# Kernel optimization log

Hardware: AMD Instinct MI355X
Metric: run time of the kernel (lower is better)

The kernel has to match this reference:

```python
import jax, jax.numpy as jnp
import numpy as np

N_NODES = 100000
N_EDGES = 6400000
NUM_FEATURES = 128
NUM_CLASSES = 10


def _gcn_norm(edge_index, num_nodes):
    # PyG GCNConv default: add self-loops, symmetric normalization
    src, dst = edge_index[0], edge_index[1]
    loop = jnp.arange(num_nodes, dtype=src.dtype)
    src = jnp.concatenate([src, loop])
    dst = jnp.concatenate([dst, loop])
    deg = jax.ops.segment_sum(jnp.ones_like(dst, dtype=jnp.float32), dst,
                              num_segments=num_nodes)
    dinv = jnp.where(deg > 0, jax.lax.rsqrt(deg), 0.0)
    norm = dinv[src] * dinv[dst]  # [E + N]
    return src, dst, norm


def _gcn_conv(x, W, b, src, dst, norm, num_nodes):
    h = x @ W                              # [N, out] small feature matmul
    msg = h[src] * norm[:, None]           # gather + per-edge scale
    agg = jax.ops.segment_sum(msg, dst, num_segments=num_nodes)  # scatter-add
    return agg + b


def setup_inputs() -> dict:
    key = jax.random.key(0)
    ks = jax.random.split(key, 10)
    x = jax.random.normal(ks[0], (N_NODES, NUM_FEATURES), dtype=jnp.float32)
    edge_index = jax.random.randint(ks[1], (2, N_EDGES), 0, N_NODES, dtype=jnp.int64)

    def glorot(k, shape):
        lim = np.sqrt(6.0 / (shape[0] + shape[1]))
        return jax.random.uniform(k, shape, jnp.float32, -lim, lim)

    return {
        "x": x,
        "edge_index": edge_index,
        "W1": glorot(ks[2], (NUM_FEATURES, 4)), "b1": jnp.zeros((4,), jnp.float32),
        "W2": glorot(ks[3], (4, 4)),            "b2": jnp.zeros((4,), jnp.float32),
        "W3": glorot(ks[4], (4, 2)),            "b3": jnp.zeros((2,), jnp.float32),
        "Wc": glorot(ks[5], (2, NUM_CLASSES)),  "bc": jnp.zeros((NUM_CLASSES,), jnp.float32),
    }


def reference(x, edge_index, W1, b1, W2, b2, W3, b3, Wc, bc):
    num_nodes = x.shape[0]
    src, dst, norm = _gcn_norm(edge_index, num_nodes)
    h = jnp.tanh(_gcn_conv(x, W1, b1, src, dst, norm, num_nodes))
    h = jnp.tanh(_gcn_conv(h, W2, b2, src, dst, norm, num_nodes))
    h = jnp.tanh(_gcn_conv(h, W3, b3, src, dst, norm, num_nodes))
    out = h @ Wc + bc
    return out, h
```

## Files before the change

kernel.cpp:

```cpp
#include <hip/hip_runtime.h>
#include <hip/hip_bf16.h>
#include <stdint.h>

#define N_NODES 100000
#define N_EDGES 6400000

#define NPB 128
#define NBKT 782
#define CAP 10752
#define SORT_CAP 9216
#define OUT_CAP (SORT_CAP + NPB * 3)
#define BIN_CHUNK 16384
#define BIN_THREADS 1024
#define SORT_THREADS 1024
#define SORT_V4 3
#define NBIN_BLOCKS ((N_EDGES + BIN_CHUNK - 1) / BIN_CHUNK)


__global__ __launch_bounds__(1024) void k_bin(const void* __restrict__ ei,
                                              int* __restrict__ gcur,
                                              unsigned* __restrict__ perm1) {
  __shared__ unsigned staging[BIN_CHUNK];
  __shared__ int lcnt[1024];
  __shared__ int combo[1024];
  __shared__ int wsum[16];
  __shared__ int s_tot;
  __shared__ int s_th[3];
  __shared__ int s_is64;
  int t = threadIdx.x;
  lcnt[t] = 0;
  if (t < 64) {
    unsigned hv = ((const unsigned*)ei)[2 * t + 1];
    unsigned long long m = __ballot(hv != 0u);
    if (t == 0) s_is64 = (m == 0ull);
  }
  __syncthreads();
  int is64 = s_is64;
  size_t e0 = (size_t)blockIdx.x * BIN_CHUNK;
  int n = (int)(((e0 + BIN_CHUNK) <= N_EDGES) ? BIN_CHUNK : (N_EDGES - e0));

  if (is64) {
    const long long* e = (const long long*)ei;
    for (int k = 2 * t; k < n; k += 2048) {
      uint4 dp = *(const uint4*)(e + (size_t)N_EDGES + e0 + k);
      if (dp.x < N_NODES) atomicAdd(&lcnt[dp.x >> 7], 1);
      if (dp.z < N_NODES) atomicAdd(&lcnt[dp.z >> 7], 1);
    }
  } else {
    const unsigned* e = (const unsigned*)ei;
    for (int k = 4 * t; k < n; k += 4096) {
      uint4 dq = *(const uint4*)(e + (size_t)N_EDGES + e0 + k);
      if (dq.x < N_NODES) atomicAdd(&lcnt[dq.x >> 7], 1);
      if (dq.y < N_NODES) atomicAdd(&lcnt[dq.y >> 7], 1);
      if (dq.z < N_NODES) atomicAdd(&lcnt[dq.z >> 7], 1);
      if (dq.w < N_NODES) atomicAdd(&lcnt[dq.w >> 7], 1);
    }
  }
  __syncthreads();
  int c = lcnt[t];
  int lane = t & 63, w = t >> 6;
  int incl = c;
#pragma unroll
  for (int o = 1; o < 64; o <<= 1) {
    int u = __shfl_up(incl, o);
    if (lane >= o) incl += u;
  }
  if (lane == 63) wsum[w] = incl;
  __syncthreads();
  int wb = 0;
  for (int i = 0; i < w; ++i) wb += wsum[i];
  int excl = wb + incl - c;
  int gb = c ? atomicAdd(&gcur[t], c) : 0;
  lcnt[t] = excl;
  combo[t] = gb - excl;
  if (t == 256) s_th[0] = excl;
  if (t == 512) s_th[1] = excl;
  if (t == 768) s_th[2] = excl;
  if (t == 1023) s_tot = excl + c;
  __syncthreads();
  if (is64) {
    const long long* e = (const long long*)ei;
    for (int k = 2 * t; k < n; k += 2048) {
      uint4 sp = *(const uint4*)(e + e0 + k);
      uint4 dp = *(const uint4*)(e + (size_t)N_EDGES + e0 + k);
      if (sp.x < N_NODES && dp.x < N_NODES) {
        int p = atomicAdd(&lcnt[dp.x >> 7], 1);
        staging[p] = sp.x | ((dp.x & (NPB - 1u)) << 17) | (((dp.x >> 7) & 255u) << 24);
      }
      if (sp.z < N_NODES && dp.z < N_NODES) {
        int p = atomicAdd(&lcnt[dp.z >> 7], 1);
        staging[p] = sp.z | ((dp.z & (NPB - 1u)) << 17) | (((dp.z >> 7) & 255u) << 24);
      }
    }
  } else {
    const unsigned* e = (const unsigned*)ei;
    for (int k = 4 * t; k < n; k += 4096) {
      uint4 sq = *(const uint4*)(e + e0 + k);
      uint4 dq = *(const uint4*)(e + (size_t)N_EDGES + e0 + k);
      if (sq.x < N_NODES && dq.x < N_NODES) {
        int p = atomicAdd(&lcnt[dq.x >> 7], 1);
        staging[p] = sq.x | ((dq.x & (NPB - 1u)) << 17) | (((dq.x >> 7) & 255u) << 24);
      }
      if (sq.y < N_NODES && dq.y < N_NODES) {
        int p = atomicAdd(&lcnt[dq.y >> 7], 1);
        staging[p] = sq.y | ((dq.y & (NPB - 1u)) << 17) | (((dq.y >> 7) & 255u) << 24);
      }
      if (sq.z < N_NODES && dq.z < N_NODES) {
        int p = atomicAdd(&lcnt[dq.z >> 7], 1);
        staging[p] = sq.z | ((dq.z & (NPB - 1u)) << 17) | (((dq.z >> 7) & 255u) << 24);
      }
      if (sq.w < N_NODES && dq.w < N_NODES) {
        int p = atomicAdd(&lcnt[dq.w >> 7], 1);
        staging[p] = sq.w | ((dq.w & (NPB - 1u)) << 17) | (((dq.w >> 7) & 255u) << 24);
      }
    }
  }
  __syncthreads();
  int tot = s_tot, th0 = s_th[0], th1 = s_th[1], th2 = s_th[2];
  for (int j = t; j < tot; j += 1024) {
    unsigned r = staging[j];
    int hi = (j >= th0) + (j >= th1) + (j >= th2);
    int b = (int)(r >> 24) | (hi << 8);
    int o = combo[b] + j;
    if (o < CAP) perm1[(size_t)b * CAP + o] = r;
  }
}

__global__ __launch_bounds__(1024) void k_sort(const int* __restrict__ gcur,
                                               const unsigned* __restrict__ perm1,
                                               unsigned* __restrict__ perm2,
                                               int2* __restrict__ offdeg,
                                               float* __restrict__ dinv) {
  __shared__ __align__(16) unsigned outbuf[OUT_CAP];
  __shared__ int h[NPB];
  __shared__ int wsum2[2];
  __shared__ int s_tot;
  int b = blockIdx.x, t = threadIdx.x;
  if (t < NPB) h[t] = 0;
  __syncthreads();
  int cnt = min(gcur[b], SORT_CAP);
  int base = b * CAP;
#pragma unroll
  for (int i = 0; i < SORT_V4; ++i) {
    int j = 4 * t + 4096 * i;
    if (j < cnt) {
      uint4 q = *(const uint4*)(perm1 + base + j);
      atomicAdd(&h[(q.x >> 17) & (NPB - 1)], 1);
      if (j + 1 < cnt) atomicAdd(&h[(q.y >> 17) & (NPB - 1)], 1);
      if (j + 2 < cnt) atomicAdd(&h[(q.z >> 17) & (NPB - 1)], 1);
      if (j + 3 < cnt) atomicAdd(&h[(q.w >> 17) & (NPB - 1)], 1);
    }
  }
  __syncthreads();
  int degb = 0, degs4 = 0, incl = 0;
  if (t < NPB) {
    degb = h[t];
    degs4 = (degb + 3) & ~3;
    incl = degs4;
    int lane = t & 63;
#pragma unroll
    for (int o = 1; o < 64; o <<= 1) {
      int u = __shfl_up(incl, o);
      if (lane >= o) incl += u;
    }
    if (lane == 63) wsum2[t >> 6] = incl;
  }
  __syncthreads();
  int excl4 = 0;
  if (t < NPB) {
    excl4 = (t >= 64 ? wsum2[0] : 0) + incl - degs4;
    int node = b * NPB + t;
    if (node < N_NODES) {
      offdeg[node] = make_int2(base + excl4, degb);
      float dd = (float)degb + 1.0f;
      float y = rsqrtf(dd);
      y = y * (1.5f - 0.5f * dd * y * y);
      dinv[node] = y;
    }
    if (t == NPB - 1) s_tot = excl4 + degs4;
  }
  __syncthreads();
  if (t < NPB) h[t] = excl4;
  __syncthreads();
#pragma unroll
  for (int i = 0; i < SORT_V4; ++i) {
    int j = 4 * t + 4096 * i;
    if (j < cnt) {
      uint4 q = *(const uint4*)(perm1 + base + j);
      { int p = atomicAdd(&h[(q.x >> 17) & (NPB - 1)], 1); outbuf[p] = q.x & 0x1FFFF; }
      if (j + 1 < cnt) { int p = atomicAdd(&h[(q.y >> 17) & (NPB - 1)], 1); outbuf[p] = q.y & 0x1FFFF; }
      if (j + 2 < cnt) { int p = atomicAdd(&h[(q.z >> 17) & (NPB - 1)], 1); outbuf[p] = q.z & 0x1FFFF; }
      if (j + 3 < cnt) { int p = atomicAdd(&h[(q.w >> 17) & (NPB - 1)], 1); outbuf[p] = q.w & 0x1FFFF; }
    }
  }
  __syncthreads();
  int tot = s_tot;
#pragma unroll
  for (int i = 0; i < SORT_V4; ++i) {
    int j = 4 * t + 4096 * i;
    if (j < tot)
      *(uint4*)(perm2 + base + j) = *(const uint4*)(outbuf + j);
  }
}

__global__ __launch_bounds__(256) void k_mm1(const float* __restrict__ x,
                                             const float* __restrict__ W1,
                                             const float* __restrict__ dinv,
                                             float* __restrict__ hs1) {
  int gid = blockIdx.x * blockDim.x + threadIdx.x;
  int node = gid >> 6;
  int lane = threadIdx.x & 63;
  if (node >= N_NODES) return;
  float2 v = ((const float2*)x)[(size_t)node * 64 + lane];
  float4 w0 = ((const float4*)W1)[2 * lane];
  float4 w1 = ((const float4*)W1)[2 * lane + 1];
  float a0 = v.x * w0.x + v.y * w1.x;
  float a1 = v.x * w0.y + v.y * w1.y;
  float a2 = v.x * w0.z + v.y * w1.z;
  float a3 = v.x * w0.w + v.y * w1.w;
#pragma unroll
  for (int off = 32; off > 0; off >>= 1) {
    a0 += __shfl_down(a0, off);
    a1 += __shfl_down(a1, off);
    a2 += __shfl_down(a2, off);
    a3 += __shfl_down(a3, off);
  }
  if (lane == 0) {
    float d = dinv[node];
    ((float4*)hs1)[node] = make_float4(d * a0, d * a1, d * a2, d * a3);
  }
}


__global__ __launch_bounds__(256) void k_l1(const int2* __restrict__ offdeg,
                                            const unsigned* __restrict__ perm2,
                                            const float* __restrict__ hs1,
                                            const float* __restrict__ dinv,
                                            const float* __restrict__ W2,
                                            const float* __restrict__ b1,
                                            float* __restrict__ hs2) {
  int node = blockIdx.x * 16 + (threadIdx.x >> 4);
  int l = threadIdx.x & 15;
  int2 od = offdeg[node];
  int base = od.x, d = od.y;
  float a0 = 0, a1 = 0, a2 = 0, a3 = 0;
  for (int j = 4 * l; j + 4 <= d; j += 64) {
    uint4 s = *(const uint4*)(perm2 + base + j);
    float4 v0 = ((const float4*)hs1)[s.x];
    float4 v1 = ((const float4*)hs1)[s.y];
    float4 v2 = ((const float4*)hs1)[s.z];
    float4 v3 = ((const float4*)hs1)[s.w];
    a0 += v0.x + v1.x + v2.x + v3.x;
    a1 += v0.y + v1.y + v2.y + v3.y;
    a2 += v0.z + v1.z + v2.z + v3.z;
    a3 += v0.w + v1.w + v2.w + v3.w;
  }
  int rb = d & ~3;
  if (l < d - rb) {
    float4 v = ((const float4*)hs1)[perm2[base + rb + l]];
    a0 += v.x; a1 += v.y; a2 += v.z; a3 += v.w;
  }
#pragma unroll
  for (int o = 8; o > 0; o >>= 1) {
    a0 += __shfl_down(a0, o); a1 += __shfl_down(a1, o);
    a2 += __shfl_down(a2, o); a3 += __shfl_down(a3, o);
  }
  if (l == 0) {
    float dn = dinv[node];
    float4 hl = ((const float4*)hs1)[node];
    float t0 = tanhf(dn * (a0 + hl.x) + b1[0]);
    float t1 = tanhf(dn * (a1 + hl.y) + b1[1]);
    float t2 = tanhf(dn * (a2 + hl.z) + b1[2]);
    float t3 = tanhf(dn * (a3 + hl.w) + b1[3]);
    float4 r;
    r.x = dn * (t0 * W2[0] + t1 * W2[4] + t2 * W2[8]  + t3 * W2[12]);
    r.y = dn * (t0 * W2[1] + t1 * W2[5] + t2 * W2[9]  + t3 * W2[13]);
    r.z = dn * (t0 * W2[2] + t1 * W2[6] + t2 * W2[10] + t3 * W2[14]);
    r.w = dn * (t0 * W2[3] + t1 * W2[7] + t2 * W2[11] + t3 * W2[15]);
    ((float4*)hs2)[node] = r;
  }
}

__global__ __launch_bounds__(256) void k_l2(const int2* __restrict__ offdeg,
                                            const unsigned* __restrict__ perm2,
                                            const float* __restrict__ hs2,
                                            const float* __restrict__ dinv,
                                            const float* __restrict__ W3,
                                            const float* __restrict__ b2,
                                            float* __restrict__ hs3) {
  int node = blockIdx.x * 16 + (threadIdx.x >> 4);
  int l = threadIdx.x & 15;
  int2 od = offdeg[node];
  int base = od.x, d = od.y;
  float a0 = 0, a1 = 0, a2 = 0, a3 = 0;
  for (int j = 4 * l; j + 4 <= d; j += 64) {
    uint4 s = *(const uint4*)(perm2 + base + j);
    float4 v0 = ((const float4*)hs2)[s.x];
    float4 v1 = ((const float4*)hs2)[s.y];
    float4 v2 = ((const float4*)hs2)[s.z];
    float4 v3 = ((const float4*)hs2)[s.w];
    a0 += v0.x + v1.x + v2.x + v3.x;
    a1 += v0.y + v1.y + v2.y + v3.y;
    a2 += v0.z + v1.z + v2.z + v3.z;
    a3 += v0.w + v1.w + v2.w + v3.w;
  }
  int rb = d & ~3;
  if (l < d - rb) {
    float4 v = ((const float4*)hs2)[perm2[base + rb + l]];
    a0 += v.x; a1 += v.y; a2 += v.z; a3 += v.w;
  }
#pragma unroll
  for (int o = 8; o > 0; o >>= 1) {
    a0 += __shfl_down(a0, o); a1 += __shfl_down(a1, o);
    a2 += __shfl_down(a2, o); a3 += __shfl_down(a3, o);
  }
  if (l == 0) {
    float dn = dinv[node];
    float4 hl = ((const float4*)hs2)[node];
    float t0 = tanhf(dn * (a0 + hl.x) + b2[0]);
    float t1 = tanhf(dn * (a1 + hl.y) + b2[1]);
    float t2 = tanhf(dn * (a2 + hl.z) + b2[2]);
    float t3 = tanhf(dn * (a3 + hl.w) + b2[3]);
    float2 r;
    r.x = dn * (t0 * W3[0] + t1 * W3[2] + t2 * W3[4] + t3 * W3[6]);
    r.y = dn * (t0 * W3[1] + t1 * W3[3] + t2 * W3[5] + t3 * W3[7]);
    ((float2*)hs3)[node] = r;
  }
}

__global__ __launch_bounds__(256) void k_l3(const int2* __restrict__ offdeg,
                                            const unsigned* __restrict__ perm2,
                                            const float* __restrict__ hs3,
                                            const float* __restrict__ dinv,
                                            const float* __restrict__ Wc,
                                            const float* __restrict__ bc,
                                            const float* __restrict__ b3,
                                            float* __restrict__ out) {
  int node = blockIdx.x * 16 + (threadIdx.x >> 4);
  int l = threadIdx.x & 15;
  int2 od = offdeg[node];
  int base = od.x, d = od.y;
  float a0 = 0, a1 = 0;
  for (int j = 4 * l; j + 4 <= d; j += 64) {
    uint4 s = *(const uint4*)(perm2 + base + j);
    float2 v0 = ((const float2*)hs3)[s.x];
    float2 v1 = ((const float2*)hs3)[s.y];
    float2 v2 = ((const float2*)hs3)[s.z];
    float2 v3 = ((const float2*)hs3)[s.w];
    a0 += v0.x + v1.x + v2.x + v3.x;
    a1 += v0.y + v1.y + v2.y + v3.y;
  }
  int rb = d & ~3;
  if (l < d - rb) {
    float2 v = ((const float2*)hs3)[perm2[base + rb + l]];
    a0 += v.x; a1 += v.y;
  }
#pragma unroll
  for (int o = 8; o > 0; o >>= 1) {
    a0 += __shfl_xor(a0, o); a1 += __shfl_xor(a1, o);
  }
  float dn = dinv[node];
  float2 hl = ((const float2*)hs3)[node];
  float t0 = tanhf(dn * (a0 + hl.x) + b3[0]);
  float t1 = tanhf(dn * (a1 + hl.y) + b3[1]);
  if (l < 10)
    out[(size_t)node * 10 + l] = t0 * Wc[l] + t1 * Wc[10 + l] + bc[l];
  else if (l == 10)
    out[(size_t)N_NODES * 10 + 2 * node + 0] = t0;
  else if (l == 11)
    out[(size_t)N_NODES * 10 + 2 * node + 1] = t1;
}

extern "C" void kernel_launch(void* const* d_in, const int* in_sizes, int n_in,
                              void* d_out, int out_size, void* d_ws, size_t ws_size,
                              hipStream_t stream) {
  const float* x  = (const float*)d_in[0];
  const void*  ei = d_in[1];
  const float* W1 = (const float*)d_in[2];
  const float* b1 = (const float*)d_in[3];
  const float* W2 = (const float*)d_in[4];
  const float* b2 = (const float*)d_in[5];
  const float* W3 = (const float*)d_in[6];
  const float* b3 = (const float*)d_in[7];
  const float* Wc = (const float*)d_in[8];
  const float* bc = (const float*)d_in[9];
  float* out = (float*)d_out;

  const size_t N = N_NODES;
  float* base = (float*)d_ws;
  float* dinv = base;
  float* hs1  = base + N;
  float* hs2  = base + 5 * N;
  float* hs3  = base + 9 * N;
  int2*  offdeg = (int2*)(base + 11 * N);
  int*   gcur = (int*)(base + 13 * N);
  unsigned* perm1 = (unsigned*)(base + 13 * N + 2048);
  unsigned* perm2 = perm1 + (size_t)NBKT * CAP;

  hipMemsetAsync(gcur, 0, 1024 * sizeof(int), stream);
  k_bin<<<NBIN_BLOCKS, BIN_THREADS, 0, stream>>>(ei, gcur, perm1);
  k_sort<<<NBKT, SORT_THREADS, 0, stream>>>(gcur, perm1, perm2, offdeg, dinv);
  k_mm1<<<(N_NODES * 64) / 256, 256, 0, stream>>>(x, W1, dinv, hs1);

  const int LB = N_NODES / 16;
  k_l1<<<LB, 256, 0, stream>>>(offdeg, perm2, hs1, dinv, W2, b1, hs2);
  k_l2<<<LB, 256, 0, stream>>>(offdeg, perm2, hs2, dinv, W3, b2, hs3);
  k_l3<<<LB, 256, 0, stream>>>(offdeg, perm2, hs3, dinv, Wc, bc, b3, out);
}
```

Baseline: 281.6 us.

## Fuse matmul and three GCN layers into one persistent kernel with grid barriers

Replaces four separate launches (x@W1 and three aggregation layers) with a single persistent kernel of 1024 blocks. The blocks use grid-stride loops and synchronize between stages through atomic-counter grid barriers held in workspace, which is zeroed by the extended memset. This removes three kernel launch gaps and their tail effects. In exchange it relies on all 1024 blocks being co-resident to avoid deadlock, and it reduces per-stage parallelism and latency hiding compared with the fully oversubscribed grids.

```diff
diff --git a/kernel.cpp b/kernel.cpp
--- a/kernel.cpp
+++ b/kernel.cpp
@@ -15,6 +15,9 @@
 #define SORT_THREADS 1024
 #define SORT_V4 3
 #define NBIN_BLOCKS ((N_EDGES + BIN_CHUNK - 1) / BIN_CHUNK)
+
+#define FUSE_BLOCKS 1024
+#define FUSE_THREADS 256
 
 
 __global__ __launch_bounds__(1024) void k_bin(const void* __restrict__ ei,
@@ -203,172 +206,176 @@
   }
 }
 
-__global__ __launch_bounds__(256) void k_mm1(const float* __restrict__ x,
-                                             const float* __restrict__ W1,
-                                             const float* __restrict__ dinv,
-                                             float* __restrict__ hs1) {
-  int gid = blockIdx.x * blockDim.x + threadIdx.x;
-  int node = gid >> 6;
-  int lane = threadIdx.x & 63;
-  if (node >= N_NODES) return;
-  float2 v = ((const float2*)x)[(size_t)node * 64 + lane];
-  float4 w0 = ((const float4*)W1)[2 * lane];
-  float4 w1 = ((const float4*)W1)[2 * lane + 1];
-  float a0 = v.x * w0.x + v.y * w1.x;
-  float a1 = v.x * w0.y + v.y * w1.y;
-  float a2 = v.x * w0.z + v.y * w1.z;
-  float a3 = v.x * w0.w + v.y * w1.w;
-#pragma unroll
-  for (int off = 32; off > 0; off >>= 1) {
-    a0 += __shfl_down(a0, off);
-    a1 += __shfl_down(a1, off);
-    a2 += __shfl_down(a2, off);
-    a3 += __shfl_down(a3, off);
-  }
-  if (lane == 0) {
-    float d = dinv[node];
-    ((float4*)hs1)[node] = make_float4(d * a0, d * a1, d * a2, d * a3);
-  }
+__device__ __forceinline__ void grid_barrier(int* bar, int id, int nb) {
+  __syncthreads();
+  if (threadIdx.x == 0) {
+    __threadfence();
+    __hip_atomic_fetch_add(&bar[id], 1, __ATOMIC_ACQ_REL, __HIP_MEMORY_SCOPE_AGENT);
+    while (__hip_atomic_load(&bar[id], __ATOMIC_ACQUIRE, __HIP_MEMORY_SCOPE_AGENT) < nb) {}
+    __threadfence();
+  }
+  __syncthreads();
 }
 
-
-__global__ __launch_bounds__(256) void k_l1(const int2* __restrict__ offdeg,
-                                            const unsigned* __restrict__ perm2,
-                                            const float* __restrict__ hs1,
-                                            const float* __restrict__ dinv,
-                                            const float* __restrict__ W2,
-                                            const float* __restrict__ b1,
-                                            float* __restrict__ hs2) {
-  int node = blockIdx.x * 16 + (threadIdx.x >> 4);
-  int l = threadIdx.x & 15;
-  int2 od = offdeg[node];
-  int base = od.x, d = od.y;
-  float a0 = 0, a1 = 0, a2 = 0, a3 = 0;
-  for (int j = 4 * l; j + 4 <= d; j += 64) {
-    uint4 s = *(const uint4*)(perm2 + base + j);
-    float4 v0 = ((const float4*)hs1)[s.x];
-    float4 v1 = ((const float4*)hs1)[s.y];
-    float4 v2 = ((const float4*)hs1)[s.z];
-    float4 v3 = ((const float4*)hs1)[s.w];
-    a0 += v0.x + v1.x + v2.x + v3.x;
-    a1 += v0.y + v1.y + v2.y + v3.y;
-    a2 += v0.z + v1.z + v2.z + v3.z;
-    a3 += v0.w + v1.w + v2.w + v3.w;
-  }
-  int rb = d & ~3;
-  if (l < d - rb) {
-    float4 v = ((const float4*)hs1)[perm2[base + rb + l]];
-    a0 += v.x; a1 += v.y; a2 += v.z; a3 += v.w;
-  }
-#pragma unroll
-  for (int o = 8; o > 0; o >>= 1) {
-    a0 += __shfl_down(a0, o); a1 += __shfl_down(a1, o);
-    a2 += __shfl_down(a2, o); a3 += __shfl_down(a3, o);
-  }
-  if (l == 0) {
+__global__ __launch_bounds__(256, 4) void k_fused(
+    const float* __restrict__ x,  const float* __restrict__ W1,
+    const int2* __restrict__ offdeg, const unsigned* __restrict__ perm2,
+    const float* __restrict__ dinv,
+    const float* __restrict__ b1, const float* __restrict__ W2,
+    const float* __restrict__ b2, const float* __restrict__ W3,
+    const float* __restrict__ b3, const float* __restrict__ Wc,
+    const float* __restrict__ bc,
+    float* __restrict__ hs1, float* __restrict__ hs2,
+    float* __restrict__ hs3, float* __restrict__ out,
+    int* __restrict__ bar) {
+  const int tid = blockIdx.x * FUSE_THREADS + threadIdx.x;
+
+  {
+    int wave = tid >> 6;
+    int lane = threadIdx.x & 63;
+    const int nwaves = (FUSE_BLOCKS * FUSE_THREADS) >> 6;
+    float4 w0 = ((const float4*)W1)[2 * lane];
+    float4 w1 = ((const float4*)W1)[2 * lane + 1];
+    for (int node = wave; node < N_NODES; node += nwaves) {
+      float2 v = ((const float2*)x)[(size_t)node * 64 + lane];
+      float a0 = v.x * w0.x + v.y * w1.x;
+      float a1 = v.x * w0.y + v.y * w1.y;
+      float a2 = v.x * w0.z + v.y * w1.z;
+      float a3 = v.x * w0.w + v.y * w1.w;
+#pragma unroll
+      for (int off = 32; off > 0; off >>= 1) {
+        a0 += __shfl_down(a0, off);
+        a1 += __shfl_down(a1, off);
+        a2 += __shfl_down(a2, off);
+        a3 += __shfl_down(a3, off);
+      }
+      if (lane == 0) {
+        float d = dinv[node];
+        ((float4*)hs1)[node] = make_float4(d * a0, d * a1, d * a2, d * a3);
+      }
+    }
+  }
+  grid_barrier(bar, 0, FUSE_BLOCKS);
+
+  const int slot = tid >> 4;
+  const int l = threadIdx.x & 15;
+  const int nslots = (FUSE_BLOCKS * FUSE_THREADS) >> 4;
+
+  for (int node = slot; node < N_NODES; node += nslots) {
+    int2 od = offdeg[node];
+    int base = od.x, d = od.y;
+    float a0 = 0, a1 = 0, a2 = 0, a3 = 0;
+    for (int j = 4 * l; j + 4 <= d; j += 64) {
+      uint4 s = *(const uint4*)(perm2 + base + j);
+      float4 v0 = ((const float4*)hs1)[s.x];
+      float4 v1 = ((const float4*)hs1)[s.y];
+      float4 v2 = ((const float4*)hs1)[s.z];
+      float4 v3 = ((const float4*)hs1)[s.w];
+      a0 += v0.x + v1.x + v2.x + v3.x;
+      a1 += v0.y + v1.y + v2.y + v3.y;
+      a2 += v0.z + v1.z + v2.z + v3.z;
+      a3 += v0.w + v1.w + v2.w + v3.w;
+    }
+    int rb = d & ~3;
+    if (l < d - rb) {
+      float4 v = ((const float4*)hs1)[perm2[base + rb + l]];
+      a0 += v.x; a1 += v.y; a2 += v.z; a3 += v.w;
+    }
+#pragma unroll
+    for (int o = 8; o > 0; o >>= 1) {
+      a0 += __shfl_down(a0, o); a1 += __shfl_down(a1, o);
+      a2 += __shfl_down(a2, o); a3 += __shfl_down(a3, o);
+    }
+    if (l == 0) {
+      float dn = dinv[node];
+      float4 hl = ((const float4*)hs1)[node];
+      float t0 = tanhf(dn * (a0 + hl.x) + b1[0]);
+      float t1 = tanhf(dn * (a1 + hl.y) + b1[1]);
+      float t2 = tanhf(dn * (a2 + hl.z) + b1[2]);
+      float t3 = tanhf(dn * (a3 + hl.w) + b1[3]);
+      float4 r;
+      r.x = dn * (t0 * W2[0] + t1 * W2[4] + t2 * W2[8]  + t3 * W2[12]);
+      r.y = dn * (t0 * W2[1] + t1 * W2[5] + t2 * W2[9]  + t3 * W2[13]);
+      r.z = dn * (t0 * W2[2] + t1 * W2[6] + t2 * W2[10] + t3 * W2[14]);
+      r.w = dn * (t0 * W2[3] + t1 * W2[7] + t2 * W2[11] + t3 * W2[15]);
+      ((float4*)hs2)[node] = r;
+    }
+  }
+  grid_barrier(bar, 1, FUSE_BLOCKS);
+
+  for (int node = slot; node < N_NODES; node += nslots) {
+    int2 od = offdeg[node];
+    int base = od.x, d = od.y;
+    float a0 = 0, a1 = 0, a2 = 0, a3 = 0;
+    for (int j = 4 * l; j + 4 <= d; j += 64) {
+      uint4 s = *(const uint4*)(perm2 + base + j);
+      float4 v0 = ((const float4*)hs2)[s.x];
+      float4 v1 = ((const float4*)hs2)[s.y];
+      float4 v2 = ((const float4*)hs2)[s.z];
+      float4 v3 = ((const float4*)hs2)[s.w];
+      a0 += v0.x + v1.x + v2.x + v3.x;
+      a1 += v0.y + v1.y + v2.y + v3.y;
+      a2 += v0.z + v1.z + v2.z + v3.z;
+      a3 += v0.w + v1.w + v2.w + v3.w;
+    }
+    int rb = d & ~3;
+    if (l < d - rb) {
+      float4 v = ((const float4*)hs2)[perm2[base + rb + l]];
+      a0 += v.x; a1 += v.y; a2 += v.z; a3 += v.w;
+    }
+#pragma unroll
+    for (int o = 8; o > 0; o >>= 1) {
+      a0 += __shfl_down(a0, o); a1 += __shfl_down(a1, o);
+      a2 += __shfl_down(a2, o); a3 += __shfl_down(a3, o);
+    }
+    if (l == 0) {
+      float dn = dinv[node];
+      float4 hl = ((const float4*)hs2)[node];
+      float t0 = tanhf(dn * (a0 + hl.x) + b2[0]);
+      float t1 = tanhf(dn * (a1 + hl.y) + b2[1]);
+      float t2 = tanhf(dn * (a2 + hl.z) + b2[2]);
+      float t3 = tanhf(dn * (a3 + hl.w) + b2[3]);
+      float2 r;
+      r.x = dn * (t0 * W3[0] + t1 * W3[2] + t2 * W3[4] + t3 * W3[6]);
+      r.y = dn * (t0 * W3[1] + t1 * W3[3] + t2 * W3[5] + t3 * W3[7]);
+      ((float2*)hs3)[node] = r;
+    }
+  }
+  grid_barrier(bar, 2, FUSE_BLOCKS);
+
+  for (int node = slot; node < N_NODES; node += nslots) {
+    int2 od = offdeg[node];
+    int base = od.x, d = od.y;
+    float a0 = 0, a1 = 0;
+    for (int j = 4 * l; j + 4 <= d; j += 64) {
+      uint4 s = *(const uint4*)(perm2 + base + j);
+      float2 v0 = ((const float2*)hs3)[s.x];
+      float2 v1 = ((const float2*)hs3)[s.y];
+      float2 v2 = ((const float2*)hs3)[s.z];
+      float2 v3 = ((const float2*)hs3)[s.w];
+      a0 += v0.x + v1.x + v2.x + v3.x;
+      a1 += v0.y + v1.y + v2.y + v3.y;
+    }
+    int rb = d & ~3;
+    if (l < d - rb) {
+      float2 v = ((const float2*)hs3)[perm2[base + rb + l]];
+      a0 += v.x; a1 += v.y;
+    }
+#pragma unroll
+    for (int o = 8; o > 0; o >>= 1) {
+      a0 += __shfl_xor(a0, o); a1 += __shfl_xor(a1, o);
+    }
     float dn = dinv[node];
-    float4 hl = ((const float4*)hs1)[node];
-    float t0 = tanhf(dn * (a0 + hl.x) + b1[0]);
-    float t1 = tanhf(dn * (a1 + hl.y) + b1[1]);
-    float t2 = tanhf(dn * (a2 + hl.z) + b1[2]);
-    float t3 = tanhf(dn * (a3 + hl.w) + b1[3]);
-    float4 r;
-    r.x = dn * (t0 * W2[0] + t1 * W2[4] + t2 * W2[8]  + t3 * W2[12]);
-    r.y = dn * (t0 * W2[1] + t1 * W2[5] + t2 * W2[9]  + t3 * W2[13]);
-    r.z = dn * (t0 * W2[2] + t1 * W2[6] + t2 * W2[10] + t3 * W2[14]);
-    r.w = dn * (t0 * W2[3] + t1 * W2[7] + t2 * W2[11] + t3 * W2[15]);
-    ((float4*)hs2)[node] = r;
-  }
-}
-
-__global__ __launch_bounds__(256) void k_l2(const int2* __restrict__ offdeg,
-                                            const unsigned* __restrict__ perm2,
-                                            const float* __restrict__ hs2,
-                                            const float* __restrict__ dinv,
-                                            const float* __restrict__ W3,
-                                            const float* __restrict__ b2,
-                                            float* __restrict__ hs3) {
-  int node = blockIdx.x * 16 + (threadIdx.x >> 4);
-  int l = threadIdx.x & 15;
-  int2 od = offdeg[node];
-  int base = od.x, d = od.y;
-  float a0 = 0, a1 = 0, a2 = 0, a3 = 0;
-  for (int j = 4 * l; j + 4 <= d; j += 64) {
-    uint4 s = *(const uint4*)(perm2 + base + j);
-    float4 v0 = ((const float4*)hs2)[s.x];
-    float4 v1 = ((const float4*)hs2)[s.y];
-    float4 v2 = ((const float4*)hs2)[s.z];
-    float4 v3 = ((const float4*)hs2)[s.w];
-    a0 += v0.x + v1.x + v2.x + v3.x;
-    a1 += v0.y + v1.y + v2.y + v3.y;
-    a2 += v0.z + v1.z + v2.z + v3.z;
-    a3 += v0.w + v1.w + v2.w + v3.w;
-  }
-  int rb = d & ~3;
-  if (l < d - rb) {
-    float4 v = ((const float4*)hs2)[perm2[base + rb + l]];
-    a0 += v.x; a1 += v.y; a2 += v.z; a3 += v.w;
-  }
-#pragma unroll
-  for (int o = 8; o > 0; o >>= 1) {
-    a0 += __shfl_down(a0, o); a1 += __shfl_down(a1, o);
-    a2 += __shfl_down(a2, o); a3 += __shfl_down(a3, o);
-  }
-  if (l == 0) {
-    float dn = dinv[node];
-    float4 hl = ((const float4*)hs2)[node];
-    float t0 = tanhf(dn * (a0 + hl.x) + b2[0]);
-    float t1 = tanhf(dn * (a1 + hl.y) + b2[1]);
-    float t2 = tanhf(dn * (a2 + hl.z) + b2[2]);
-    float t3 = tanhf(dn * (a3 + hl.w) + b2[3]);
-    float2 r;
-    r.x = dn * (t0 * W3[0] + t1 * W3[2] + t2 * W3[4] + t3 * W3[6]);
-    r.y = dn * (t0 * W3[1] + t1 * W3[3] + t2 * W3[5] + t3 * W3[7]);
-    ((float2*)hs3)[node] = r;
-  }
-}
-
-__global__ __launch_bounds__(256) void k_l3(const int2* __restrict__ offdeg,
-                                            const unsigned* __restrict__ perm2,
-                                            const float* __restrict__ hs3,
-                                            const float* __restrict__ dinv,
-                                            const float* __restrict__ Wc,
-                                            const float* __restrict__ bc,
-                                            const float* __restrict__ b3,
-                                            float* __restrict__ out) {
-  int node = blockIdx.x * 16 + (threadIdx.x >> 4);
-  int l = threadIdx.x & 15;
-  int2 od = offdeg[node];
-  int base = od.x, d = od.y;
-  float a0 = 0, a1 = 0;
-  for (int j = 4 * l; j + 4 <= d; j += 64) {
-    uint4 s = *(const uint4*)(perm2 + base + j);
-    float2 v0 = ((const float2*)hs3)[s.x];
-    float2 v1 = ((const float2*)hs3)[s.y];
-    float2 v2 = ((const float2*)hs3)[s.z];
-    float2 v3 = ((const float2*)hs3)[s.w];
-    a0 += v0.x + v1.x + v2.x + v3.x;
-    a1 += v0.y + v1.y + v2.y + v3.y;
-  }
-  int rb = d & ~3;
-  if (l < d - rb) {
-    float2 v = ((const float2*)hs3)[perm2[base + rb + l]];
-    a0 += v.x; a1 += v.y;
-  }
-#pragma unroll
-  for (int o = 8; o > 0; o >>= 1) {
-    a0 += __shfl_xor(a0, o); a1 += __shfl_xor(a1, o);
-  }
-  float dn = dinv[node];
-  float2 hl = ((const float2*)hs3)[node];
-  float t0 = tanhf(dn * (a0 + hl.x) + b3[0]);
-  float t1 = tanhf(dn * (a1 + hl.y) + b3[1]);
-  if (l < 10)
-    out[(size_t)node * 10 + l] = t0 * Wc[l] + t1 * Wc[10 + l] + bc[l];
-  else if (l == 10)
-    out[(size_t)N_NODES * 10 + 2 * node + 0] = t0;
-  else if (l == 11)
-    out[(size_t)N_NODES * 10 + 2 * node + 1] = t1;
+    float2 hl = ((const float2*)hs3)[node];
+    float t0 = tanhf(dn * (a0 + hl.x) + b3[0]);
+    float t1 = tanhf(dn * (a1 + hl.y) + b3[1]);
+    if (l < 10)
+      out[(size_t)node * 10 + l] = t0 * Wc[l] + t1 * Wc[10 + l] + bc[l];
+    else if (l == 10)
+      out[(size_t)N_NODES * 10 + 2 * node + 0] = t0;
+    else if (l == 11)
+      out[(size_t)N_NODES * 10 + 2 * node + 1] = t1;
+  }
 }
 
 extern "C" void kernel_launch(void* const* d_in, const int* in_sizes, int n_in,
@@ -394,16 +401,14 @@
   float* hs3  = base + 9 * N;
   int2*  offdeg = (int2*)(base + 11 * N);
   int*   gcur = (int*)(base + 13 * N);
+  int*   bar  = (int*)(base + 13 * N + 1024);
   unsigned* perm1 = (unsigned*)(base + 13 * N + 2048);
   unsigned* perm2 = perm1 + (size_t)NBKT * CAP;
 
-  hipMemsetAsync(gcur, 0, 1024 * sizeof(int), stream);
+  hipMemsetAsync(gcur, 0, (1024 + 16) * sizeof(int), stream);
   k_bin<<<NBIN_BLOCKS, BIN_THREADS, 0, stream>>>(ei, gcur, perm1);
   k_sort<<<NBKT, SORT_THREADS, 0, stream>>>(gcur, perm1, perm2, offdeg, dinv);
-  k_mm1<<<(N_NODES * 64) / 256, 256, 0, stream>>>(x, W1, dinv, hs1);
-
-  const int LB = N_NODES / 16;
-  k_l1<<<LB, 256, 0, stream>>>(offdeg, perm2, hs1, dinv, W2, b1, hs2);
-  k_l2<<<LB, 256, 0, stream>>>(offdeg, perm2, hs2, dinv, W3, b2, hs3);
-  k_l3<<<LB, 256, 0, stream>>>(offdeg, perm2, hs3, dinv, Wc, bc, b3, out);
+  k_fused<<<FUSE_BLOCKS, FUSE_THREADS, 0, stream>>>(
+      x, W1, offdeg, perm2, dinv, b1, W2, b2, W3, b3, Wc, bc,
+      hs1, hs2, hs3, out, bar);
 }
```

After: 843.5 us. +199.5%, slower.
